# Kernel tuning notes

Hardware: AMD Instinct MI355X
Metric: run time of the kernel (lower is better)

## Reference

```python
import jax, jax.numpy as jnp
import numpy as np

PI = 3.1415927410125732
N = 4096
VELOCITY = 5e-7
RC = 3.15e-6          # collision radius
RR = 8e-6             # repulsion radius
RO = 2.5e-5           # orientation radius (Ra = inf -> inside_Ra all-true)
ALPHA = PI            # field of view; < 2*pi so within_view masking is active
DT_TRANS = 1.4e-14    # translational diffusion DT
DR = 0.0028
GAMMA = 25.0
DT = 0.2              # timestep dt
COLLISION_ITERS = 3   # fixed-iteration version of recursive solve_collisions
EPS = 1e-14


def _c(x):  # [N,2] real -> complex64
    return jax.lax.complex(x[..., 0], x[..., 1])


def _r(z):  # complex -> [..., 2] real
    return jnp.stack([z.real, z.imag], axis=-1)


def _anglediff(a, b):
    # torch get_anglediff: wrap angle(a)-angle(b) into (-pi, pi)
    diff = jnp.angle(a) - jnp.angle(b)
    diff = jnp.where(diff <= -PI, jnp.mod(diff, PI), diff)
    return diff - (diff >= PI) * (2.0 * PI)


def _cossim(a, b):
    # nn.CosineSimilarity(dim=1, eps=1e-14) on view_as_real of complex vectors
    dot = a.real * b.real + a.imag * b.imag
    na = jnp.sqrt(a.real ** 2 + a.imag ** 2 + 1e-30)
    nb = jnp.sqrt(b.real ** 2 + b.imag ** 2 + 1e-30)
    return dot / (jnp.maximum(na, EPS) * jnp.maximum(nb, EPS))


def setup_inputs() -> dict:
    key = jax.random.key(0)
    k1, k2, k3, k4, k5 = jax.random.split(key, 5)
    positions = jax.random.normal(k1, (N, 2), jnp.float32) * 5e-4
    ang = jax.random.uniform(k2, (N,), jnp.float32, -PI, PI)
    orientations = jnp.stack([jnp.cos(ang), jnp.sin(ang)], axis=-1)  # unit complex
    Deltas = jax.random.uniform(k3, (1,), jnp.float32, 0.1, 0.6)
    rot_noise = jax.random.normal(k4, (N,), jnp.float32)
    trans_noise = jax.random.normal(k5, (N, 2), jnp.float32)
    return {"positions": positions, "orientations": orientations, "Deltas": Deltas,
            "rot_noise": rot_noise, "trans_noise": trans_noise}


def reference(positions, orientations, Deltas, rot_noise, trans_noise):
    p = _c(positions)      # [N] complex positions
    u = _c(orientations)   # [N] complex orientations
    n = p.shape[0]
    eye = jnp.eye(n, dtype=bool)

    # pairwise direction/distance: dirs[i,j] = p_j - p_i
    dirs = p[None, :] - p[:, None]
    dists = jnp.abs(dirs)

    inside_Rr = (dists <= RR) & ~eye
    inside_Ro = dists <= RO + RC
    # inside_Ra with Ra = inf is all-True

    # angle between separation vector and orientation of the *neighbor* j
    ang_diff = _anglediff(dirs, u[None, :])
    in_front = ang_diff < PI / 2
    within_view = ang_diff < ALPHA  # alpha < 2*pi branch active

    cdtype = p.dtype
    mask_rr = (inside_Rr & in_front).astype(cdtype)
    mask_ra = within_view.astype(cdtype)  # inside_Ra all True
    mask_ro = (inside_Ro & within_view).astype(cdtype)

    n_r = mask_rr.real.sum(axis=1)
    S = (mask_rr @ p) / jnp.maximum(n_r, 1.0) - p * jnp.sign(n_r)
    d = -S

    n_a = mask_ra.real.sum(axis=1)
    cms = (mask_ra @ p) / jnp.maximum(n_a, 1.0)
    Ps = cms - p * jnp.sign(n_a)

    orientation_sums = mask_ro @ u

    leftturns = Ps * jnp.exp(1j * Deltas)
    rightturns = Ps * jnp.exp(-1j * Deltas)

    # T >= T_release branch: pick the turn most aligned with neighbor orientations
    left_closer = _cossim(leftturns, orientation_sums) >= _cossim(rightturns, orientation_sums)
    best_turns = jnp.where(left_closer, leftturns, rightturns)

    d_abs = jnp.abs(d)
    d_safe = jnp.where(d_abs > 0, d, jnp.ones((), cdtype))
    best_safe = jnp.where(jnp.abs(best_turns) > 0, best_turns, jnp.ones((), cdtype))
    angle_to_target = jnp.where(d_abs > 0, _anglediff(d_safe, u), _anglediff(best_safe, u))

    # rotational_noise = randn * sqrt(2*DR); rotation = exp(i*(dt*Gamma*DR*sin + noise*sqrt(dt)))
    rot = jnp.exp(1j * (DT * GAMMA * DR * jnp.sin(angle_to_target)
                        + rot_noise * np.float32(np.sqrt(2 * DR)) * np.float32(np.sqrt(DT))))

    # complex-normal translational noise (per-component std 1/sqrt(2)) * sqrt(2*DT) * sqrt(dt)
    tn = _c(trans_noise) * np.float32(np.sqrt(0.5)) * np.float32(np.sqrt(2 * DT_TRANS))
    translation = DT * VELOCITY * u + tn * np.float32(np.sqrt(DT))

    def collide(i, pos):
        dd = pos[None, :] - pos[:, None]
        dd_nd = jnp.where(eye, jnp.ones((), pos.dtype), dd)  # avoid 0/0 on diagonal
        ab = jnp.where(eye, 0.0, jnp.abs(dd_nd))
        coll = ab <= 2 * RC - jnp.eye(n, dtype=ab.dtype)
        safe = jnp.where(coll, ab, 1.0)
        move = jnp.where(coll, dd / safe * ((2.1 * RC - ab) * 0.5), jnp.zeros((), pos.dtype))
        return pos - move.sum(axis=1)

    new_p = jax.lax.fori_loop(0, COLLISION_ITERS, collide, p + translation)
    new_u = u * rot

    # pack the 5 complex outputs as real [5, N, 2]
    return jnp.stack([_r(new_p), _r(new_u), _r(orientation_sums), _r(leftturns), _r(rightturns)], axis=0)
```

## Files before the change

### kernel.cpp

```cpp
#include <hip/hip_runtime.h>
#include <math.h>

#define NPART 4096
#define NBLK  512
#define NTHR  256
#define IPB   8
#define CAP   512
#define MAXP  (NBLK * CAP)
#define KREG  32

constexpr float RORC   = (float)(2.5e-5 + 3.15e-6);
constexpr float RORC2  = RORC * RORC;
constexpr float RRF    = 8e-6f;
constexpr float RR2    = RRF * RRF;
constexpr float TWORC  = (float)(2.0 * 3.15e-6);
constexpr float TWORC2 = TWORC * TWORC;
constexpr float C21RC  = (float)(2.1 * 3.15e-6);
constexpr float RCAND2 = 1.6e-9f;
constexpr float C_ROT  = (float)(0.2 * 25.0 * 0.0028);
constexpr float C_RN1  = (float)0.07483314773547883;
constexpr float C_SQDT = (float)0.4472135954999579;
constexpr float C_TRV  = (float)(0.2 * 5e-7);
constexpr float C_HALF = (float)0.7071067811865476;
constexpr float C_SQ2T = (float)1.6733200530681511e-07;
constexpr float EPSF   = 1e-14f;

__global__ void zero_counter(int* __restrict__ counter) {
    *counter = 0;
}

__global__ __launch_bounds__(NTHR) void fused_main(
        const float2* __restrict__ pos, const float2* __restrict__ ori,
        const float* __restrict__ Deltas, const float* __restrict__ rot_noise,
        const float2* __restrict__ trans_noise,
        float2* __restrict__ out, float2* __restrict__ pA,
        int* __restrict__ counter, int* __restrict__ pairs_g) {
    __shared__ float4 pp4[NPART / 2];
    __shared__ float2 pori_s[NPART];
    __shared__ float  sred[5 * NTHR];
    __shared__ float  res[5][IPB];
    __shared__ int    lcnt, lbase;
    __shared__ int    lpairs[CAP];
    float2* ppos_s = (float2*)pp4;

    const int tid  = threadIdx.x;
    if (tid == 0) lcnt = 0;
    const int il   = tid & (IPB - 1);
    const int seg  = tid / IPB;
    const int gi   = blockIdx.x * IPB + il;
    const int base = seg * 128;

    for (int k = 0; k < NPART / NTHR; ++k) {
        const int j = k * NTHR + tid;
        ppos_s[j] = pos[j];
        pori_s[j] = ori[j];
    }
    __syncthreads();

    const float2 pi = ppos_s[gi];
    float nr = 0.f, sx = 0.f, sy = 0.f, oxs = 0.f, oys = 0.f;
    #pragma unroll 4
    for (int t = 0; t < 64; ++t) {
        const int k2 = (t + seg) & 63;
        const int j0 = base + 2 * k2;
        const float4 v = pp4[j0 >> 1];
        const float dx0 = v.x - pi.x, dy0 = v.y - pi.y;
        const float dx1 = v.z - pi.x, dy1 = v.w - pi.y;
        const float r20 = fmaf(dx0, dx0, dy0 * dy0);
        const float r21 = fmaf(dx1, dx1, dy1 * dy1);
        if (r20 <= RCAND2) {
            const float2 uj = pori_s[j0];
            if (r20 <= RORC2) { oxs += uj.x; oys += uj.y; }
            if (r20 > 0.f) {
                if (r20 <= RR2) {
                    const float dt_ = fmaf(dx0, uj.x, dy0 * uj.y);
                    const float cr_ = fmaf(dy0, uj.x, -dx0 * uj.y);
                    if (!((dt_ <= 0.f) && (cr_ >= 0.f))) { nr += 1.f; sx += v.x; sy += v.y; }
                }
                const int slot = atomicAdd(&lcnt, 1);
                if (slot < CAP) lpairs[slot] = (gi << 12) | j0;
            }
        }
        if (r21 <= RCAND2) {
            const int j1 = j0 + 1;
            const float2 uj = pori_s[j1];
            if (r21 <= RORC2) { oxs += uj.x; oys += uj.y; }
            if (r21 > 0.f) {
                if (r21 <= RR2) {
                    const float dt_ = fmaf(dx1, uj.x, dy1 * uj.y);
                    const float cr_ = fmaf(dy1, uj.x, -dx1 * uj.y);
                    if (!((dt_ <= 0.f) && (cr_ >= 0.f))) { nr += 1.f; sx += v.z; sy += v.w; }
                }
                const int slot = atomicAdd(&lcnt, 1);
                if (slot < CAP) lpairs[slot] = (gi << 12) | j1;
            }
        }
    }
    __syncthreads();
    sred[0 * NTHR + tid] = nr;
    sred[1 * NTHR + tid] = sx;
    sred[2 * NTHR + tid] = sy;
    sred[3 * NTHR + tid] = oxs;
    sred[4 * NTHR + tid] = oys;
    if (tid == 0) {
        const int n_l = (lcnt < CAP) ? lcnt : CAP;
        lbase = atomicAdd(counter, n_l);
        lcnt  = n_l;
    }
    __syncthreads();
    if (tid < 5 * IPB) {
        const int q = tid / IPB, ii = tid & (IPB - 1);
        float acc = 0.f;
        #pragma unroll
        for (int s = 0; s < 32; ++s) acc += sred[q * NTHR + ii + IPB * s];
        res[q][ii] = acc;
    }
    for (int e = tid; e < lcnt; e += NTHR)
        pairs_g[lbase + e] = lpairs[e];
    __syncthreads();

    float mx = 0.f, my = 0.f;
    for (int k = 0; k < NPART / NTHR; ++k) {
        const float2 v = ppos_s[k * NTHR + tid];
        mx += v.x; my += v.y;
    }
    sred[tid] = mx; sred[NTHR + tid] = my;
    __syncthreads();
    for (int s = NTHR / 2; s > 0; s >>= 1) {
        if (tid < s) { sred[tid] += sred[tid + s]; sred[NTHR + tid] += sred[NTHR + tid + s]; }
        __syncthreads();
    }
    const float cmx = sred[0]    * (1.f / NPART);
    const float cmy = sred[NTHR] * (1.f / NPART);

    if (tid < IPB) {
        const int g2 = blockIdx.x * IPB + tid;
        const float2 p = ppos_s[g2];
        const float2 u = pori_s[g2];
        const float nrv = res[0][tid], sxv = res[1][tid], syv = res[2][tid];
        const float osx = res[3][tid], osy = res[4][tid];

        const float inv = 1.f / fmaxf(nrv, 1.f);
        const float sg  = (nrv > 0.f) ? 1.f : 0.f;
        const float Sx = sxv * inv - p.x * sg;
        const float Sy = syv * inv - p.y * sg;
        const float dxv = -Sx, dyv = -Sy;

        const float Psx = cmx - p.x;
        const float Psy = cmy - p.y;

        float sd, cd;
        sincosf(Deltas[0], &sd, &cd);
        const float Lx = Psx * cd - Psy * sd;
        const float Ly = Psx * sd + Psy * cd;
        const float Rx = Psx * cd + Psy * sd;
        const float Ry = Psy * cd - Psx * sd;

        const float no  = fmaxf(sqrtf(osx * osx + osy * osy + 1e-30f), EPSF);
        const float nl  = fmaxf(sqrtf(Lx * Lx + Ly * Ly + 1e-30f), EPSF);
        const float nrr = fmaxf(sqrtf(Rx * Rx + Ry * Ry + 1e-30f), EPSF);
        const float csl = (Lx * osx + Ly * osy) / (nl * no);
        const float csr = (Rx * osx + Ry * osy) / (nrr * no);
        const bool left = (csl >= csr);
        const float bx = left ? Lx : Rx;
        const float by = left ? Ly : Ry;

        float cx, cy;
        if (dxv != 0.f || dyv != 0.f)    { cx = dxv; cy = dyv; }
        else if (bx != 0.f || by != 0.f) { cx = bx;  cy = by;  }
        else                             { cx = 1.f; cy = 0.f; }

        const float dt_ = cx * u.x + cy * u.y;
        const float cr_ = cy * u.x - cx * u.y;
        const float sin_t = cr_ / sqrtf(dt_ * dt_ + cr_ * cr_);

        const float ang = C_ROT * sin_t + (rot_noise[g2] * C_RN1) * C_SQDT;
        float sa, ca;
        sincosf(ang, &sa, &ca);
        const float nux = u.x * ca - u.y * sa;
        const float nuy = u.x * sa + u.y * ca;

        const float2 tn = trans_noise[g2];
        const float tvx = C_TRV * u.x + ((tn.x * C_HALF) * C_SQ2T) * C_SQDT;
        const float tvy = C_TRV * u.y + ((tn.y * C_HALF) * C_SQ2T) * C_SQDT;

        out[1 * NPART + g2] = make_float2(nux, nuy);
        out[2 * NPART + g2] = make_float2(osx, osy);
        out[3 * NPART + g2] = make_float2(Lx, Ly);
        out[4 * NPART + g2] = make_float2(Rx, Ry);
        pA[g2] = make_float2(p.x + tvx, p.y + tvy);
    }
}

__global__ __launch_bounds__(1024) void collide_sparse(
        const float2* __restrict__ pA, const int* __restrict__ counter,
        const int* __restrict__ pairs_g, float2* __restrict__ out0) {
    __shared__ float2 ppos[NPART];
    __shared__ float  macx[NPART];
    __shared__ float  macy[NPART];

    const int tid = threadIdx.x;
    for (int k = 0; k < NPART / 1024; ++k)
        ppos[k * 1024 + tid] = pA[k * 1024 + tid];
    int nc = *counter;
    nc = (nc < KREG * 1024) ? nc : KREG * 1024;

    int pk[KREG];
    #pragma unroll
    for (int k = 0; k < KREG; ++k) {
        const int e = tid + k * 1024;
        pk[k] = (e < nc) ? pairs_g[e] : -1;
    }
    __syncthreads();

    for (int pass = 0; pass < 3; ++pass) {
        for (int k = 0; k < NPART / 1024; ++k) {
            macx[k * 1024 + tid] = 0.f;
            macy[k * 1024 + tid] = 0.f;
        }
        __syncthreads();
        #pragma unroll
        for (int k = 0; k < KREG; ++k) {
            if (pk[k] >= 0) {
                const int i = pk[k] >> 12;
                const int j = pk[k] & (NPART - 1);
                const float2 pi = ppos[i];
                const float2 pj = ppos[j];
                const float dx = pj.x - pi.x, dy = pj.y - pi.y;
                const float r2 = fmaf(dx, dx, dy * dy);
                if (r2 <= TWORC2 && r2 > 0.f) {
                    const float ab = sqrtf(r2);
                    const float s = (C21RC - ab) * 0.5f / ab;
                    atomicAdd(&macx[i], dx * s);
                    atomicAdd(&macy[i], dy * s);
                }
            }
        }
        __syncthreads();
        for (int k = 0; k < NPART / 1024; ++k) {
            const int i = k * 1024 + tid;
            ppos[i].x -= macx[i];
            ppos[i].y -= macy[i];
        }
        __syncthreads();
    }
    for (int k = 0; k < NPART / 1024; ++k)
        out0[k * 1024 + tid] = ppos[k * 1024 + tid];
}

extern "C" void kernel_launch(void* const* d_in, const int* in_sizes, int n_in,
                              void* d_out, int out_size, void* d_ws, size_t ws_size,
                              hipStream_t stream) {
    const float2* pos = (const float2*)d_in[0];
    const float2* ori = (const float2*)d_in[1];
    const float*  del = (const float*)d_in[2];
    const float*  rn  = (const float*)d_in[3];
    const float2* tn  = (const float2*)d_in[4];

    float2* pA      = (float2*)d_ws;
    int*    counter = (int*)((char*)d_ws + NPART * sizeof(float2));
    int*    pairs   = counter + 16;
    float2* o2      = (float2*)d_out;

    zero_counter<<<dim3(1), dim3(1), 0, stream>>>(counter);
    fused_main<<<dim3(NBLK), dim3(NTHR), 0, stream>>>(pos, ori, del, rn, tn,
                                                      o2, pA, counter, pairs);
    collide_sparse<<<dim3(1), dim3(1024), 0, stream>>>(pA, counter, pairs, o2);
}
```

Baseline: 103.1 us.

## Deduplicate collision pairs, use per-block pair slots, drop counter-reset kernel

Only pairs with i<j are recorded, and the collision kernel applies the displacement symmetrically to both particles, halving the pair work. Each block writes its pairs into a fixed per-block slot with a count, so the global atomic counter and the separate zero-counter launch go away. The single-block collide kernel scans the counts and compacts the pairs into shared memory. Displacements are now atomically added straight into the shared positions during a pass instead of into separate accumulators. That mixes updated and old positions within an iteration, which departs from the simultaneous update in the reference.

```diff
diff --git a/kernel.cpp b/kernel.cpp
--- a/kernel.cpp
+++ b/kernel.cpp
@@ -6,8 +6,7 @@
 #define NTHR  256
 #define IPB   8
 #define CAP   512
-#define MAXP  (NBLK * CAP)
-#define KREG  32
+#define FCAP  16384
 
 constexpr float RORC   = (float)(2.5e-5 + 3.15e-6);
 constexpr float RORC2  = RORC * RORC;
@@ -25,21 +24,17 @@
 constexpr float C_SQ2T = (float)1.6733200530681511e-07;
 constexpr float EPSF   = 1e-14f;
 
-__global__ void zero_counter(int* __restrict__ counter) {
-    *counter = 0;
-}
-
 __global__ __launch_bounds__(NTHR) void fused_main(
         const float2* __restrict__ pos, const float2* __restrict__ ori,
         const float* __restrict__ Deltas, const float* __restrict__ rot_noise,
         const float2* __restrict__ trans_noise,
         float2* __restrict__ out, float2* __restrict__ pA,
-        int* __restrict__ counter, int* __restrict__ pairs_g) {
+        int* __restrict__ counts_g, int* __restrict__ pairs_g) {
     __shared__ float4 pp4[NPART / 2];
     __shared__ float2 pori_s[NPART];
     __shared__ float  sred[5 * NTHR];
     __shared__ float  res[5][IPB];
-    __shared__ int    lcnt, lbase;
+    __shared__ int    lcnt;
     __shared__ int    lpairs[CAP];
     float2* ppos_s = (float2*)pp4;
 
@@ -77,8 +72,10 @@
                     const float cr_ = fmaf(dy0, uj.x, -dx0 * uj.y);
                     if (!((dt_ <= 0.f) && (cr_ >= 0.f))) { nr += 1.f; sx += v.x; sy += v.y; }
                 }
-                const int slot = atomicAdd(&lcnt, 1);
-                if (slot < CAP) lpairs[slot] = (gi << 12) | j0;
+                if (gi < j0) {
+                    const int slot = atomicAdd(&lcnt, 1);
+                    if (slot < CAP) lpairs[slot] = (gi << 12) | j0;
+                }
             }
         }
         if (r21 <= RCAND2) {
@@ -91,8 +88,10 @@
                     const float cr_ = fmaf(dy1, uj.x, -dx1 * uj.y);
                     if (!((dt_ <= 0.f) && (cr_ >= 0.f))) { nr += 1.f; sx += v.z; sy += v.w; }
                 }
-                const int slot = atomicAdd(&lcnt, 1);
-                if (slot < CAP) lpairs[slot] = (gi << 12) | j1;
+                if (gi < j1) {
+                    const int slot = atomicAdd(&lcnt, 1);
+                    if (slot < CAP) lpairs[slot] = (gi << 12) | j1;
+                }
             }
         }
     }
@@ -102,11 +101,6 @@
     sred[2 * NTHR + tid] = sy;
     sred[3 * NTHR + tid] = oxs;
     sred[4 * NTHR + tid] = oys;
-    if (tid == 0) {
-        const int n_l = (lcnt < CAP) ? lcnt : CAP;
-        lbase = atomicAdd(counter, n_l);
-        lcnt  = n_l;
-    }
     __syncthreads();
     if (tid < 5 * IPB) {
         const int q = tid / IPB, ii = tid & (IPB - 1);
@@ -115,8 +109,12 @@
         for (int s = 0; s < 32; ++s) acc += sred[q * NTHR + ii + IPB * s];
         res[q][ii] = acc;
     }
-    for (int e = tid; e < lcnt; e += NTHR)
-        pairs_g[lbase + e] = lpairs[e];
+    {
+        const int n_l = (lcnt < CAP) ? lcnt : CAP;
+        for (int e = tid; e < n_l; e += NTHR)
+            pairs_g[blockIdx.x * CAP + e] = lpairs[e];
+        if (tid == 0) counts_g[blockIdx.x] = n_l;
+    }
     __syncthreads();
 
     float mx = 0.f, my = 0.f;
@@ -193,54 +191,61 @@
 }
 
 __global__ __launch_bounds__(1024) void collide_sparse(
-        const float2* __restrict__ pA, const int* __restrict__ counter,
+        const float2* __restrict__ pA, const int* __restrict__ counts_g,
         const int* __restrict__ pairs_g, float2* __restrict__ out0) {
     __shared__ float2 ppos[NPART];
-    __shared__ float  macx[NPART];
-    __shared__ float  macy[NPART];
+    __shared__ int    flat[FCAP];
+    __shared__ int    scan[NBLK];
 
     const int tid = threadIdx.x;
     for (int k = 0; k < NPART / 1024; ++k)
         ppos[k * 1024 + tid] = pA[k * 1024 + tid];
-    int nc = *counter;
-    nc = (nc < KREG * 1024) ? nc : KREG * 1024;
-
-    int pk[KREG];
-    #pragma unroll
-    for (int k = 0; k < KREG; ++k) {
-        const int e = tid + k * 1024;
-        pk[k] = (e < nc) ? pairs_g[e] : -1;
+
+    int c_own = 0;
+    if (tid < NBLK) {
+        c_own = counts_g[tid];
+        scan[tid] = c_own;
+    }
+    __syncthreads();
+    for (int off = 1; off < NBLK; off <<= 1) {
+        int v = 0;
+        if (tid < NBLK) {
+            v = scan[tid];
+            if (tid >= off) v += scan[tid - off];
+        }
+        __syncthreads();
+        if (tid < NBLK) scan[tid] = v;
+        __syncthreads();
+    }
+    const int total_raw = scan[NBLK - 1];
+    const int total = (total_raw < FCAP) ? total_raw : FCAP;
+    if (tid < NBLK) {
+        const int off = scan[tid] - c_own;
+        for (int e = 0; e < c_own; ++e) {
+            const int idx = off + e;
+            if (idx < FCAP) flat[idx] = pairs_g[tid * CAP + e];
+        }
     }
     __syncthreads();
 
     for (int pass = 0; pass < 3; ++pass) {
-        for (int k = 0; k < NPART / 1024; ++k) {
-            macx[k * 1024 + tid] = 0.f;
-            macy[k * 1024 + tid] = 0.f;
-        }
-        __syncthreads();
-        #pragma unroll
-        for (int k = 0; k < KREG; ++k) {
-            if (pk[k] >= 0) {
-                const int i = pk[k] >> 12;
-                const int j = pk[k] & (NPART - 1);
-                const float2 pi = ppos[i];
-                const float2 pj = ppos[j];
-                const float dx = pj.x - pi.x, dy = pj.y - pi.y;
-                const float r2 = fmaf(dx, dx, dy * dy);
-                if (r2 <= TWORC2 && r2 > 0.f) {
-                    const float ab = sqrtf(r2);
-                    const float s = (C21RC - ab) * 0.5f / ab;
-                    atomicAdd(&macx[i], dx * s);
-                    atomicAdd(&macy[i], dy * s);
-                }
+        for (int e = tid; e < total; e += 1024) {
+            const int code = flat[e];
+            const int i = code >> 12;
+            const int j = code & (NPART - 1);
+            const float2 pi = ppos[i];
+            const float2 pj = ppos[j];
+            const float dx = pj.x - pi.x, dy = pj.y - pi.y;
+            const float r2 = fmaf(dx, dx, dy * dy);
+            if (r2 <= TWORC2 && r2 > 0.f) {
+                const float ab = sqrtf(r2);
+                const float s = (C21RC - ab) * 0.5f / ab;
+                const float mx = dx * s, my = dy * s;
+                atomicAdd(&ppos[i].x, -mx);
+                atomicAdd(&ppos[i].y, -my);
+                atomicAdd(&ppos[j].x,  mx);
+                atomicAdd(&ppos[j].y,  my);
             }
-        }
-        __syncthreads();
-        for (int k = 0; k < NPART / 1024; ++k) {
-            const int i = k * 1024 + tid;
-            ppos[i].x -= macx[i];
-            ppos[i].y -= macy[i];
         }
         __syncthreads();
     }
@@ -257,13 +262,12 @@
     const float*  rn  = (const float*)d_in[3];
     const float2* tn  = (const float2*)d_in[4];
 
-    float2* pA      = (float2*)d_ws;
-    int*    counter = (int*)((char*)d_ws + NPART * sizeof(float2));
-    int*    pairs   = counter + 16;
-    float2* o2      = (float2*)d_out;
-
-    zero_counter<<<dim3(1), dim3(1), 0, stream>>>(counter);
+    float2* pA     = (float2*)d_ws;
+    int*    counts = (int*)((char*)d_ws + NPART * sizeof(float2));
+    int*    pairs  = counts + NBLK;
+    float2* o2     = (float2*)d_out;
+
     fused_main<<<dim3(NBLK), dim3(NTHR), 0, stream>>>(pos, ori, del, rn, tn,
-                                                      o2, pA, counter, pairs);
-    collide_sparse<<<dim3(1), dim3(1024), 0, stream>>>(pA, counter, pairs, o2);
+                                                      o2, pA, counts, pairs);
+    collide_sparse<<<dim3(1), dim3(1024), 0, stream>>>(pA, counts, pairs, o2);
 }
```

Result: faster. 98.49 us (-4.5%).

## Fuse collision solve into main kernel via per-block local neighbourhood recomputation

Applied to the files above, without the earlier changes.

Removes the counter-zeroing kernel and the single-block global collision kernel. Each block now marks a bitmap of its own particles' neighbours within a candidate radius, gathers that local set into shared memory and runs the three collision passes redundantly on it, then writes only its own particles' final positions. This drops two launches, the global pair list and a serial single-workgroup stage, in exchange for duplicated O(S^2) work per block. It assumes three collision iterations never propagate beyond the candidate radius and that each set fits within SMAX.

```diff
diff --git a/kernel.cpp b/kernel.cpp
--- a/kernel.cpp
+++ b/kernel.cpp
@@ -5,9 +5,7 @@
 #define NBLK  512
 #define NTHR  256
 #define IPB   8
-#define CAP   512
-#define MAXP  (NBLK * CAP)
-#define KREG  32
+#define SMAX  512
 
 constexpr float RORC   = (float)(2.5e-5 + 3.15e-6);
 constexpr float RORC2  = RORC * RORC;
@@ -25,26 +23,24 @@
 constexpr float C_SQ2T = (float)1.6733200530681511e-07;
 constexpr float EPSF   = 1e-14f;
 
-__global__ void zero_counter(int* __restrict__ counter) {
-    *counter = 0;
-}
-
-__global__ __launch_bounds__(NTHR) void fused_main(
+__global__ __launch_bounds__(NTHR) void fused_all(
         const float2* __restrict__ pos, const float2* __restrict__ ori,
         const float* __restrict__ Deltas, const float* __restrict__ rot_noise,
-        const float2* __restrict__ trans_noise,
-        float2* __restrict__ out, float2* __restrict__ pA,
-        int* __restrict__ counter, int* __restrict__ pairs_g) {
-    __shared__ float4 pp4[NPART / 2];
-    __shared__ float2 pori_s[NPART];
-    __shared__ float  sred[5 * NTHR];
-    __shared__ float  res[5][IPB];
-    __shared__ int    lcnt, lbase;
-    __shared__ int    lpairs[CAP];
+        const float2* __restrict__ trans_noise, float2* __restrict__ out) {
+    __shared__ float4   pp4[NPART / 2];
+    __shared__ float2   pori_s[NPART];
+    __shared__ float    sred[5 * NTHR];
+    __shared__ float    res[5][IPB];
+    __shared__ unsigned bmap[NPART / 32];
+    __shared__ int      Sidx[SMAX];
+    __shared__ float2   posS[SMAX];
+    __shared__ int      scnt;
+    __shared__ int      iloc[IPB];
     float2* ppos_s = (float2*)pp4;
 
     const int tid  = threadIdx.x;
-    if (tid == 0) lcnt = 0;
+    if (tid == 0) scnt = 0;
+    if (tid < NPART / 32) bmap[tid] = 0u;
     const int il   = tid & (IPB - 1);
     const int seg  = tid / IPB;
     const int gi   = blockIdx.x * IPB + il;
@@ -77,8 +73,7 @@
                     const float cr_ = fmaf(dy0, uj.x, -dx0 * uj.y);
                     if (!((dt_ <= 0.f) && (cr_ >= 0.f))) { nr += 1.f; sx += v.x; sy += v.y; }
                 }
-                const int slot = atomicAdd(&lcnt, 1);
-                if (slot < CAP) lpairs[slot] = (gi << 12) | j0;
+                atomicOr(&bmap[j0 >> 5], 1u << (j0 & 31));
             }
         }
         if (r21 <= RCAND2) {
@@ -91,22 +86,18 @@
                     const float cr_ = fmaf(dy1, uj.x, -dx1 * uj.y);
                     if (!((dt_ <= 0.f) && (cr_ >= 0.f))) { nr += 1.f; sx += v.z; sy += v.w; }
                 }
-                const int slot = atomicAdd(&lcnt, 1);
-                if (slot < CAP) lpairs[slot] = (gi << 12) | j1;
-            }
-        }
-    }
+                atomicOr(&bmap[j1 >> 5], 1u << (j1 & 31));
+            }
+        }
+    }
+    if (tid < IPB)
+        atomicOr(&bmap[gi >> 5], 1u << (gi & 31));
     __syncthreads();
     sred[0 * NTHR + tid] = nr;
     sred[1 * NTHR + tid] = sx;
     sred[2 * NTHR + tid] = sy;
     sred[3 * NTHR + tid] = oxs;
     sred[4 * NTHR + tid] = oys;
-    if (tid == 0) {
-        const int n_l = (lcnt < CAP) ? lcnt : CAP;
-        lbase = atomicAdd(counter, n_l);
-        lcnt  = n_l;
-    }
     __syncthreads();
     if (tid < 5 * IPB) {
         const int q = tid / IPB, ii = tid & (IPB - 1);
@@ -115,9 +106,22 @@
         for (int s = 0; s < 32; ++s) acc += sred[q * NTHR + ii + IPB * s];
         res[q][ii] = acc;
     }
-    for (int e = tid; e < lcnt; e += NTHR)
-        pairs_g[lbase + e] = lpairs[e];
-    __syncthreads();
+    if (tid >= 64 && tid < 64 + NPART / 32) {
+        const int w = tid - 64;
+        unsigned bits = bmap[w];
+        while (bits) {
+            const int b = __ffs(bits) - 1;
+            bits &= bits - 1;
+            const int p = w * 32 + b;
+            const int slot = atomicAdd(&scnt, 1);
+            if (slot < SMAX) {
+                Sidx[slot] = p;
+                if ((p >> 3) == (int)blockIdx.x) iloc[p & (IPB - 1)] = slot;
+            }
+        }
+    }
+    __syncthreads();
+    const int nS = (scnt < SMAX) ? scnt : SMAX;
 
     float mx = 0.f, my = 0.f;
     for (int k = 0; k < NPART / NTHR; ++k) {
@@ -132,6 +136,16 @@
     }
     const float cmx = sred[0]    * (1.f / NPART);
     const float cmy = sred[NTHR] * (1.f / NPART);
+
+    for (int m = tid; m < nS; m += NTHR) {
+        const int p = Sidx[m];
+        const float2 pp = ppos_s[p];
+        const float2 uu = pori_s[p];
+        const float2 tn = trans_noise[p];
+        posS[m] = make_float2(
+            pp.x + (C_TRV * uu.x + ((tn.x * C_HALF) * C_SQ2T) * C_SQDT),
+            pp.y + (C_TRV * uu.y + ((tn.y * C_HALF) * C_SQ2T) * C_SQDT));
+    }
 
     if (tid < IPB) {
         const int g2 = blockIdx.x * IPB + tid;
@@ -180,72 +194,48 @@
         const float nux = u.x * ca - u.y * sa;
         const float nuy = u.x * sa + u.y * ca;
 
-        const float2 tn = trans_noise[g2];
-        const float tvx = C_TRV * u.x + ((tn.x * C_HALF) * C_SQ2T) * C_SQDT;
-        const float tvy = C_TRV * u.y + ((tn.y * C_HALF) * C_SQ2T) * C_SQDT;
-
         out[1 * NPART + g2] = make_float2(nux, nuy);
         out[2 * NPART + g2] = make_float2(osx, osy);
         out[3 * NPART + g2] = make_float2(Lx, Ly);
         out[4 * NPART + g2] = make_float2(Rx, Ry);
-        pA[g2] = make_float2(p.x + tvx, p.y + tvy);
-    }
-}
-
-__global__ __launch_bounds__(1024) void collide_sparse(
-        const float2* __restrict__ pA, const int* __restrict__ counter,
-        const int* __restrict__ pairs_g, float2* __restrict__ out0) {
-    __shared__ float2 ppos[NPART];
-    __shared__ float  macx[NPART];
-    __shared__ float  macy[NPART];
-
-    const int tid = threadIdx.x;
-    for (int k = 0; k < NPART / 1024; ++k)
-        ppos[k * 1024 + tid] = pA[k * 1024 + tid];
-    int nc = *counter;
-    nc = (nc < KREG * 1024) ? nc : KREG * 1024;
-
-    int pk[KREG];
-    #pragma unroll
-    for (int k = 0; k < KREG; ++k) {
-        const int e = tid + k * 1024;
-        pk[k] = (e < nc) ? pairs_g[e] : -1;
     }
     __syncthreads();
 
     for (int pass = 0; pass < 3; ++pass) {
-        for (int k = 0; k < NPART / 1024; ++k) {
-            macx[k * 1024 + tid] = 0.f;
-            macy[k * 1024 + tid] = 0.f;
+        float ax[2] = {0.f, 0.f}, ay[2] = {0.f, 0.f};
+        float px[2], py[2];
+        #pragma unroll
+        for (int q = 0; q < 2; ++q) {
+            const int m = tid + q * NTHR;
+            if (m < nS) { px[q] = posS[m].x; py[q] = posS[m].y; }
+        }
+        for (int b = 0; b < nS; ++b) {
+            const float2 pb = posS[b];
+            #pragma unroll
+            for (int q = 0; q < 2; ++q) {
+                const int m = tid + q * NTHR;
+                if (m < nS) {
+                    const float dx = pb.x - px[q], dy = pb.y - py[q];
+                    const float r2 = fmaf(dx, dx, dy * dy);
+                    if (r2 <= TWORC2 && r2 > 0.f) {
+                        const float ab = sqrtf(r2);
+                        const float s = (C21RC - ab) * 0.5f / ab;
+                        ax[q] = fmaf(dx, s, ax[q]);
+                        ay[q] = fmaf(dy, s, ay[q]);
+                    }
+                }
+            }
         }
         __syncthreads();
         #pragma unroll
-        for (int k = 0; k < KREG; ++k) {
-            if (pk[k] >= 0) {
-                const int i = pk[k] >> 12;
-                const int j = pk[k] & (NPART - 1);
-                const float2 pi = ppos[i];
-                const float2 pj = ppos[j];
-                const float dx = pj.x - pi.x, dy = pj.y - pi.y;
-                const float r2 = fmaf(dx, dx, dy * dy);
-                if (r2 <= TWORC2 && r2 > 0.f) {
-                    const float ab = sqrtf(r2);
-                    const float s = (C21RC - ab) * 0.5f / ab;
-                    atomicAdd(&macx[i], dx * s);
-                    atomicAdd(&macy[i], dy * s);
-                }
-            }
+        for (int q = 0; q < 2; ++q) {
+            const int m = tid + q * NTHR;
+            if (m < nS) posS[m] = make_float2(px[q] - ax[q], py[q] - ay[q]);
         }
         __syncthreads();
-        for (int k = 0; k < NPART / 1024; ++k) {
-            const int i = k * 1024 + tid;
-            ppos[i].x -= macx[i];
-            ppos[i].y -= macy[i];
-        }
-        __syncthreads();
-    }
-    for (int k = 0; k < NPART / 1024; ++k)
-        out0[k * 1024 + tid] = ppos[k * 1024 + tid];
+    }
+    if (tid < IPB)
+        out[0 * NPART + blockIdx.x * IPB + tid] = posS[iloc[tid]];
 }
 
 extern "C" void kernel_launch(void* const* d_in, const int* in_sizes, int n_in,
@@ -256,14 +246,8 @@
     const float*  del = (const float*)d_in[2];
     const float*  rn  = (const float*)d_in[3];
     const float2* tn  = (const float2*)d_in[4];
-
-    float2* pA      = (float2*)d_ws;
-    int*    counter = (int*)((char*)d_ws + NPART * sizeof(float2));
-    int*    pairs   = counter + 16;
-    float2* o2      = (float2*)d_out;
-
-    zero_counter<<<dim3(1), dim3(1), 0, stream>>>(counter);
-    fused_main<<<dim3(NBLK), dim3(NTHR), 0, stream>>>(pos, ori, del, rn, tn,
-                                                      o2, pA, counter, pairs);
-    collide_sparse<<<dim3(1), dim3(1024), 0, stream>>>(pA, counter, pairs, o2);
+    float2* o2 = (float2*)d_out;
+    (void)d_ws; (void)ws_size;
+
+    fused_all<<<dim3(NBLK), dim3(NTHR), 0, stream>>>(pos, ori, del, rn, tn, o2);
 }
```

Measured after the change: 102.0 us. About the same (-1.1%).
